# Performance work log

Measured on AMD Instinct MI355X. Metric: run time of the kernel, lower is better.

Reference implementation:

```python
import jax, jax.numpy as jnp
import numpy as np
from jax import lax

B, C, H, W = 16, 512, 64, 64
DIM_OUT = C
IN_CH = DIM_OUT * 2          # 1024
OUT_CH = DIM_OUT // 2 * 3    # 768
ATT_DIM = DIM_OUT // 2       # 256
DN = ('NCHW', 'OIHW', 'NCHW')


def setup_inputs() -> dict:
    key = jax.random.key(0)
    k = jax.random.split(key, 6)
    x = jax.random.normal(k[0], (B, C, H, W), dtype=jnp.float32)
    y = jax.random.normal(k[1], (B, C, H, W), dtype=jnp.float32)
    # DSConv = depthwise 3x3 (groups=IN_CH) + pointwise 1x1, both with bias.
    dw_w = jax.random.normal(k[2], (IN_CH, 1, 3, 3), dtype=jnp.float32) * 0.05
    dw_b = jax.random.normal(k[3], (IN_CH,), dtype=jnp.float32) * 0.02
    pw_w = jax.random.normal(k[4], (OUT_CH, IN_CH, 1, 1), dtype=jnp.float32) * 0.02
    pw_b = jax.random.normal(k[5], (OUT_CH,), dtype=jnp.float32) * 0.02
    return {"x": x, "y": y, "dw_w": dw_w, "dw_b": dw_b, "pw_w": pw_w, "pw_b": pw_b}


def reference(x, y, dw_w, dw_b, pw_w, pw_b):
    b, c, h, w = x.shape
    inp = jnp.concatenate([x, y], axis=1)  # [b, 2c, h, w]
    # depthwise 3x3, padding=1
    t = lax.conv_general_dilated(inp, dw_w, (1, 1), 'SAME',
                                 dimension_numbers=DN,
                                 feature_group_count=IN_CH)
    t = t + dw_b[None, :, None, None]
    # pointwise 1x1
    fm = lax.conv_general_dilated(t, pw_w, (1, 1), 'SAME', dimension_numbers=DN)
    fm = fm + pw_b[None, :, None, None]                      # [b, 3*att, h, w]
    # rearrange 'b (qkv c) h w -> qkv b h c w'
    qkv = fm.reshape(b, 3, ATT_DIM, h, w).transpose(1, 0, 3, 2, 4)  # [3,b,h,c,w]
    Q, K, V = qkv[0], qkv[1], qkv[2]                         # each [b,h,c,w]
    dots = jnp.einsum('bhcw,bhdw->bhcd', Q, K)               # unscaled, [b,h,c,c]
    attn = jax.nn.softmax(dots, axis=-1)
    out = jnp.einsum('bhcd,bhdw->bhcw', attn, V)             # [b,h,c,w]
    # torch .view(b, -1, h, w): plain row-major reshape of [b,h,c,w]
    return out.reshape(b, -1, h, w)                          # [b, c, h, w]
```

## Files before the change

kernel.cpp:

```cpp
#include <hip/hip_runtime.h>

typedef unsigned short u16;
typedef float f32x4 __attribute__((ext_vector_type(4)));
typedef short s16x8 __attribute__((ext_vector_type(8)));
typedef _Float16 f16x8 __attribute__((ext_vector_type(8)));

static __device__ __forceinline__ u16 f2h(float f) {
  return __builtin_bit_cast(u16, (_Float16)f);
}

static __device__ __forceinline__ f32x4 MFMA(s16x8 a, s16x8 b, f32x4 c) {
  return __builtin_amdgcn_mfma_f32_16x16x32_f16(
      __builtin_bit_cast(f16x8, a), __builtin_bit_cast(f16x8, b), c, 0, 0, 0);
}

static __device__ __forceinline__ void g2l16(const u16* g, u16* l) {
  __builtin_amdgcn_global_load_lds(
      (const __attribute__((address_space(1))) void*)g,
      (__attribute__((address_space(3))) void*)l, 16, 0, 0);
}

__global__ __launch_bounds__(256) void convw_kernel(
    const float* __restrict__ w, u16* __restrict__ wb) {
  const int i = (blockIdx.x * 256 + threadIdx.x) * 4;
  const f32x4 v = *(const f32x4*)(w + i);
  ushort4 o;
  o.x = f2h(v.x); o.y = f2h(v.y); o.z = f2h(v.z); o.w = f2h(v.w);
  *(ushort4*)(wb + i) = o;
}

__global__ __launch_bounds__(256, 4) void dwconv_kernel(
    const float* __restrict__ x, const float* __restrict__ y,
    const float* __restrict__ dww, const float* __restrict__ dwb,
    u16* __restrict__ Tt) {
  __shared__ __align__(16) u16 tile[4][64][68];
  __shared__ float wl[640];
  const int icb = blockIdx.x, hb = blockIdx.y, b = blockIdx.z;
  const int t = threadIdx.x;

  for (int i = t; i < 576; i += 256) wl[i] = dww[icb * 576 + i];
  if (t < 64) wl[576 + t] = dwb[icb * 64 + t];
  __syncthreads();

  const int wq = t & 15;
  const int cs = t >> 4;
  const int h0 = hb * 4;

#pragma unroll
  for (int cc = 0; cc < 4; ++cc) {
    const int ch = cs * 4 + cc;
    const int ic = icb * 64 + ch;
    const float* src = (ic < 512) ? (x + (size_t)(b * 512 + ic) * 4096)
                                  : (y + (size_t)(b * 512 + (ic - 512)) * 4096);
    f32x4 r[6];
    float lm[6], lp[6];
#pragma unroll
    for (int j = 0; j < 6; ++j) {
      const int hh = h0 - 1 + j;
      f32x4 v = {0.f, 0.f, 0.f, 0.f};
      if (hh >= 0 && hh <= 63) v = *(const f32x4*)(src + hh * 64 + wq * 4);
      r[j] = v;
      const float l = __shfl_up(v.w, 1, 16);
      const float rr = __shfl_down(v.x, 1, 16);
      lm[j] = (wq == 0) ? 0.f : l;
      lp[j] = (wq == 15) ? 0.f : rr;
    }
    const float w00 = wl[ch * 9 + 0], w01 = wl[ch * 9 + 1], w02 = wl[ch * 9 + 2];
    const float w10 = wl[ch * 9 + 3], w11 = wl[ch * 9 + 4], w12 = wl[ch * 9 + 5];
    const float w20 = wl[ch * 9 + 6], w21 = wl[ch * 9 + 7], w22 = wl[ch * 9 + 8];
    const float bias = wl[576 + ch];
#pragma unroll
    for (int ro = 0; ro < 4; ++ro) {
      f32x4 acc = {bias, bias, bias, bias};
#pragma unroll
      for (int d = 0; d < 3; ++d) {
        const int j = ro + d;
        const float wa = (d == 0) ? w00 : (d == 1) ? w10 : w20;
        const float wb_ = (d == 0) ? w01 : (d == 1) ? w11 : w21;
        const float wc = (d == 0) ? w02 : (d == 1) ? w12 : w22;
        acc.x += wa * lm[j]   + wb_ * r[j].x + wc * r[j].y;
        acc.y += wa * r[j].x  + wb_ * r[j].y + wc * r[j].z;
        acc.z += wa * r[j].y  + wb_ * r[j].z + wc * r[j].w;
        acc.w += wa * r[j].z  + wb_ * r[j].w + wc * lp[j];
      }
      ushort4 o;
      o.x = f2h(acc.x); o.y = f2h(acc.y); o.z = f2h(acc.z); o.w = f2h(acc.w);
      *(ushort4*)&tile[ro][ch][wq * 4] = o;
    }
  }
  __syncthreads();

  const int icq = t & 15;
  const size_t outb = (size_t)b * 4096 * 1024 + (size_t)icb * 64 + icq * 4;
#pragma unroll
  for (int it = 0; it < 16; ++it) {
    const int ro = it >> 2;
    const int w = (it & 3) * 16 + (t >> 4);
    ushort4 o;
    o.x = tile[ro][icq * 4 + 0][w];
    o.y = tile[ro][icq * 4 + 1][w];
    o.z = tile[ro][icq * 4 + 2][w];
    o.w = tile[ro][icq * 4 + 3][w];
    const size_t p = (size_t)(h0 + ro) * 64 + w;
    *(ushort4*)(Tt + outb + p * 1024) = o;
  }
}

__global__ __launch_bounds__(256) void pwgemm_kernel(
    const u16* __restrict__ W, const float* __restrict__ pwb,
    const u16* __restrict__ Tt, u16* __restrict__ FM) {
  __shared__ __align__(16) u16 sA[128 * 64];
  __shared__ __align__(16) u16 sB[128 * 64];
  const int b = blockIdx.z;
  const int m0 = blockIdx.y * 128, n0 = blockIdx.x * 128;
  const int t = threadIdx.x, wv = t >> 6, lane = t & 63;
  const int mw = (wv >> 1) * 64, nw = (wv & 1) * 64;
  const int l15 = lane & 15, lq = lane >> 4;
  const int rsw = (l15 & 7) << 3;
  f32x4 acc[4][4] = {};
  const int r8 = lane >> 3;
  const int colsw = 8 * ((lane & 7) ^ r8);
  const u16* gA = W + ((size_t)m0 + wv * 8 + r8) * 1024 + colsw;
  const u16* gB = Tt + ((size_t)b * 4096 + n0 + wv * 8 + r8) * 1024 + colsw;
  u16* lA = sA + wv * 512;
  u16* lB = sB + wv * 512;
  for (int k0 = 0; k0 < 1024; k0 += 64) {
    __syncthreads();
#pragma unroll
    for (int jj = 0; jj < 4; ++jj) {
      g2l16(gA + (size_t)jj * 32 * 1024 + k0, lA + jj * 2048);
      g2l16(gB + (size_t)jj * 32 * 1024 + k0, lB + jj * 2048);
    }
    __syncthreads();
#pragma unroll
    for (int ks = 0; ks < 2; ++ks) {
      s16x8 af[4], bfv[4];
      const int cbase = (ks * 32 + lq * 8) ^ rsw;
#pragma unroll
      for (int i = 0; i < 4; ++i)
        af[i] = *(const s16x8*)&sA[(mw + i * 16 + l15) * 64 + cbase];
#pragma unroll
      for (int j = 0; j < 4; ++j)
        bfv[j] = *(const s16x8*)&sB[(nw + j * 16 + l15) * 64 + cbase];
#pragma unroll
      for (int i = 0; i < 4; ++i)
#pragma unroll
        for (int j = 0; j < 4; ++j)
          acc[i][j] = MFMA(af[i], bfv[j], acc[i][j]);
    }
  }
#pragma unroll
  for (int i = 0; i < 4; ++i)
#pragma unroll
    for (int r = 0; r < 4; ++r) {
      const int oc = m0 + mw + i * 16 + lq * 4 + r;
      const float bias = pwb[oc];
#pragma unroll
      for (int j = 0; j < 4; ++j) {
        const int p = n0 + nw + j * 16 + l15;
        FM[((size_t)b * 768 + oc) * 4096 + p] = f2h(acc[i][j][r] + bias);
      }
    }
}

__global__ __launch_bounds__(256) void attn_kernel(
    const u16* __restrict__ FM, float* __restrict__ out) {
  __shared__ __align__(16) u16 sKV[16384];
  __shared__ __align__(16) u16 sP[16384];
  const int sb = blockIdx.x, h = blockIdx.y, b = blockIdx.z;
  const int t = threadIdx.x, wv = t >> 6, lane = t & 63;
  const int l15 = lane & 15, lq = lane >> 4;
  const int rsw = (l15 & 7) << 3;
  const u16* fmb = FM + (size_t)b * 768 * 4096;
  const int hofs = h * 64;

  const int r8 = lane >> 3;
  const int colsw = 8 * ((lane & 7) ^ r8);
  const u16* gK = fmb + ((size_t)(256 + wv * 8 + r8)) * 4096 + hofs + colsw;
  u16* lK = sKV + wv * 512;
#pragma unroll
  for (int it = 0; it < 8; ++it)
    g2l16(gK + (size_t)it * 32 * 4096, lK + it * 2048);

  const int qrow = sb * 64 + wv * 16 + l15;
  s16x8 qf[2];
#pragma unroll
  for (int ks = 0; ks < 2; ++ks)
    qf[ks] = *(const s16x8*)(fmb + (size_t)qrow * 4096 + hofs + ks * 32 + lq * 8);
  __syncthreads();

  f32x4 sreg[16] = {};
#pragma unroll
  for (int ks = 0; ks < 2; ++ks) {
    const int cbase = (ks * 32 + lq * 8) ^ rsw;
#pragma unroll
    for (int j = 0; j < 16; ++j) {
      const s16x8 kf = *(const s16x8*)&sKV[(j * 16 + l15) * 64 + cbase];
      sreg[j] = MFMA(qf[ks], kf, sreg[j]);
    }
  }

  float inv[4], mx[4];
#pragma unroll
  for (int r = 0; r < 4; ++r) {
    float v = -3.4e38f;
#pragma unroll
    for (int j = 0; j < 16; ++j) v = fmaxf(v, sreg[j][r]);
#pragma unroll
    for (int mk = 1; mk < 16; mk <<= 1) v = fmaxf(v, __shfl_xor(v, mk, 64));
    mx[r] = v;
  }
#pragma unroll
  for (int r = 0; r < 4; ++r) {
    float ss = 0.f;
#pragma unroll
    for (int j = 0; j < 16; ++j) {
      const float e = __expf(fminf(sreg[j][r] - mx[r], 0.f));
      sreg[j][r] = e;
      ss += e;
    }
#pragma unroll
    for (int mk = 1; mk < 16; mk <<= 1) ss += __shfl_xor(ss, mk, 64);
    inv[r] = 1.0f / fmaxf(ss, 1e-30f);
  }
#pragma unroll
  for (int r = 0; r < 4; ++r) {
    const int row = wv * 16 + lq * 4 + r;
    const int s = (row & 7) << 3;
#pragma unroll
    for (int j = 0; j < 16; ++j)
      sP[row * 256 + ((j * 16 + l15) ^ s)] = f2h(sreg[j][r] * inv[r]);
  }
  __syncthreads();

#pragma unroll
  for (int it = 0; it < 8; ++it) {
    const int c = it * 256 + t;
    const int d = c >> 3, w0 = (c & 7) * 8;
    const s16x8 vv = *(const s16x8*)(fmb + (size_t)(512 + d) * 4096 + hofs + w0);
#pragma unroll
    for (int j = 0; j < 8; ++j) {
      const int rr = w0 + j;
      const int s = ((rr & 7) ^ ((rr >> 3) & 7)) << 3;
      sKV[rr * 256 + (d ^ s)] = (u16)vv[j];
    }
  }
  __syncthreads();

  f32x4 o[4] = {};
#pragma unroll
  for (int kk = 0; kk < 8; ++kk) {
    const int cbase = kk * 32 + lq * 8;
    const s16x8 pf = *(const s16x8*)&sP[(wv * 16 + l15) * 256 + (cbase ^ rsw)];
#pragma unroll
    for (int j = 0; j < 4; ++j) {
      const int rr = j * 16 + l15;
      const int vsw = ((rr & 7) ^ ((rr >> 3) & 7)) << 3;
      const s16x8 vf = *(const s16x8*)&sKV[rr * 256 + (cbase ^ vsw)];
      o[j] = MFMA(pf, vf, o[j]);
    }
  }
  const size_t ob = (((size_t)b * 64 + h) * 256 + sb * 64 + wv * 16) * 64;
#pragma unroll
  for (int j = 0; j < 4; ++j)
#pragma unroll
    for (int r = 0; r < 4; ++r)
      out[ob + (size_t)(lq * 4 + r) * 64 + j * 16 + l15] = o[j][r];
}

extern "C" void kernel_launch(void* const* d_in, const int* in_sizes, int n_in,
                              void* d_out, int out_size, void* d_ws, size_t ws_size,
                              hipStream_t stream) {
  (void)in_sizes; (void)n_in; (void)out_size; (void)ws_size;
  const float* x   = (const float*)d_in[0];
  const float* y   = (const float*)d_in[1];
  const float* dww = (const float*)d_in[2];
  const float* dwb = (const float*)d_in[3];
  const float* pww = (const float*)d_in[4];
  const float* pwb = (const float*)d_in[5];
  u16* Tt   = (u16*)d_ws;
  u16* FM   = Tt + (size_t)16 * 4096 * 1024;
  u16* Wb16 = FM + (size_t)16 * 768 * 4096;
  float* out = (float*)d_out;

  convw_kernel<<<dim3(768), 256, 0, stream>>>(pww, Wb16);
  dwconv_kernel<<<dim3(16, 16, 16), 256, 0, stream>>>(x, y, dww, dwb, Tt);
  pwgemm_kernel<<<dim3(32, 6, 16), 256, 0, stream>>>(Wb16, pwb, Tt, FM);
  attn_kernel<<<dim3(4, 64, 16), 256, 0, stream>>>(FM, out);
}
```

Before: 532.9 us.

## Double-buffer pointwise GEMM LDS tiles and remap attention block order

The pointwise GEMM now keeps two LDS buffers per operand and prefetches the next K tile with direct global-to-LDS loads while the current tile feeds the MFMAs. Explicit vmcnt waits and raw barriers replace the two __syncthreads per iteration, so load latency overlaps with compute. The attention kernel also remaps the linear block index so that consecutive blocks are spread across XCDs in an interleaved order, aiming for better L2 locality across the four sub-blocks of each (b,h). LDS use in the GEMM doubles to 64KB, which may lower occupancy, and the hand-written waitcnt depends on how many loads are still in flight.

```diff
diff --git a/kernel.cpp b/kernel.cpp
--- a/kernel.cpp
+++ b/kernel.cpp
@@ -109,8 +109,8 @@
 __global__ __launch_bounds__(256) void pwgemm_kernel(
     const u16* __restrict__ W, const float* __restrict__ pwb,
     const u16* __restrict__ Tt, u16* __restrict__ FM) {
-  __shared__ __align__(16) u16 sA[128 * 64];
-  __shared__ __align__(16) u16 sB[128 * 64];
+  __shared__ __align__(16) u16 sA[2][128 * 64];
+  __shared__ __align__(16) u16 sB[2][128 * 64];
   const int b = blockIdx.z;
   const int m0 = blockIdx.y * 128, n0 = blockIdx.x * 128;
   const int t = threadIdx.x, wv = t >> 6, lane = t & 63;
@@ -122,26 +122,39 @@
   const int colsw = 8 * ((lane & 7) ^ r8);
   const u16* gA = W + ((size_t)m0 + wv * 8 + r8) * 1024 + colsw;
   const u16* gB = Tt + ((size_t)b * 4096 + n0 + wv * 8 + r8) * 1024 + colsw;
-  u16* lA = sA + wv * 512;
-  u16* lB = sB + wv * 512;
-  for (int k0 = 0; k0 < 1024; k0 += 64) {
-    __syncthreads();
-#pragma unroll
-    for (int jj = 0; jj < 4; ++jj) {
-      g2l16(gA + (size_t)jj * 32 * 1024 + k0, lA + jj * 2048);
-      g2l16(gB + (size_t)jj * 32 * 1024 + k0, lB + jj * 2048);
-    }
-    __syncthreads();
+  const int lofs = wv * 512;
+
+#pragma unroll
+  for (int jj = 0; jj < 4; ++jj) {
+    g2l16(gA + (size_t)jj * 32 * 1024, &sA[0][lofs + jj * 2048]);
+    g2l16(gB + (size_t)jj * 32 * 1024, &sB[0][lofs + jj * 2048]);
+  }
+  for (int kt = 0; kt < 16; ++kt) {
+    const int cur = kt & 1;
+    __builtin_amdgcn_s_barrier();
+    if (kt < 15) {
+      const int k1 = (kt + 1) * 64, nxt = cur ^ 1;
+#pragma unroll
+      for (int jj = 0; jj < 4; ++jj) {
+        g2l16(gA + (size_t)jj * 32 * 1024 + k1, &sA[nxt][lofs + jj * 2048]);
+        g2l16(gB + (size_t)jj * 32 * 1024 + k1, &sB[nxt][lofs + jj * 2048]);
+      }
+      asm volatile("s_waitcnt vmcnt(8)" ::: "memory");
+    } else {
+      asm volatile("s_waitcnt vmcnt(0)" ::: "memory");
+    }
+    __builtin_amdgcn_s_barrier();
+    __builtin_amdgcn_sched_barrier(0);
 #pragma unroll
     for (int ks = 0; ks < 2; ++ks) {
       s16x8 af[4], bfv[4];
       const int cbase = (ks * 32 + lq * 8) ^ rsw;
 #pragma unroll
       for (int i = 0; i < 4; ++i)
-        af[i] = *(const s16x8*)&sA[(mw + i * 16 + l15) * 64 + cbase];
+        af[i] = *(const s16x8*)&sA[cur][(mw + i * 16 + l15) * 64 + cbase];
 #pragma unroll
       for (int j = 0; j < 4; ++j)
-        bfv[j] = *(const s16x8*)&sB[(nw + j * 16 + l15) * 64 + cbase];
+        bfv[j] = *(const s16x8*)&sB[cur][(nw + j * 16 + l15) * 64 + cbase];
 #pragma unroll
       for (int i = 0; i < 4; ++i)
 #pragma unroll
@@ -167,7 +180,9 @@
     const u16* __restrict__ FM, float* __restrict__ out) {
   __shared__ __align__(16) u16 sKV[16384];
   __shared__ __align__(16) u16 sP[16384];
-  const int sb = blockIdx.x, h = blockIdx.y, b = blockIdx.z;
+  const int lin = blockIdx.x + 4 * (blockIdx.y + 64 * blockIdx.z);
+  const int lg = (lin & 7) * 512 + (lin >> 3);
+  const int sb = lg & 3, h = (lg >> 2) & 63, b = lg >> 8;
   const int t = threadIdx.x, wv = t >> 6, lane = t & 63;
   const int l15 = lane & 15, lq = lane >> 4;
   const int rsw = (l15 & 7) << 3;
```

After: 526.7 us. Within noise of the previous version (-1.2%).
